# Kernel tuning notes

Hardware: AMD Instinct MI355X
Metric: run time of the kernel (lower is better)

## Reference

```python
import jax, jax.numpy as jnp
import numpy as np

B, V, N = 64, 64, 16384
R, Y = 32, 32          # obs_vocab, y_classes
HID = 128
BIG = 1.0e9


def _features(tables, sigma, base_obs, actions, responses, t):
    """Vectorized version of _score_one_step over the whole batch.

    tables: [B,V,N] int32 in [0,R); sigma: [B,N] int32 in [0,Y).
    Returns feat [B, V+1, 2] = stack([exp_amb, exp_sz], -1).
    """
    # candidate mask cand0 from base_obs and the (action, response) prefix
    m = tables[:, 0, :] == base_obs[:, None]                  # [B,N]
    used = jnp.zeros((B, V), dtype=bool)
    for i in range(t):
        a = actions[:, i]
        is_stop = a == V
        ac = jnp.clip(a, 0, V - 1)
        lbl = jnp.take_along_axis(tables, ac[:, None, None], axis=1)[:, 0, :]  # [B,N]
        m = m & (is_stop[:, None] | (lbl == responses[:, i][:, None]))
        used = used.at[jnp.arange(B), ac].max(~is_stop)
    mf = m.astype(jnp.float32)
    total0 = mf.sum(-1)                                       # [B]
    safe_tot = jnp.maximum(total0, 1.0)

    # per-(batch, action, response) bucket counts: counts[b,a,r] = |{n : cand0 & tables[b,a,n]==r}|
    b_ix = jnp.arange(B)[:, None, None]
    a_ix = jnp.arange(V)[None, :, None]
    flat = (b_ix * V + a_ix) * R + tables                     # [B,V,N]
    w = jnp.broadcast_to(mf[:, None, :], (B, V, N)).ravel()
    counts = jnp.zeros((B * V * R,), jnp.float32).at[flat.ravel()].add(w).reshape(B, V, R)

    # per-bucket distinct sigma values: presence[b,a,r,y] = 1 if some candidate in bucket has sigma==y
    flat2 = flat * Y + sigma[:, None, :]                      # [B,V,N]
    pres = jnp.zeros((B * V * R * Y,), jnp.float32).at[flat2.ravel()].max(w).reshape(B, V, R, Y)
    uniq = pres.sum(-1)                                       # [B,V,R]

    # expected size / ambiguity: sum_r (sz_r/total0)*sz_r and (sz_r/total0)*uniq_r
    exp_sz = (counts * counts).sum(-1) / safe_tot[:, None]    # [B,V]
    exp_amb = (counts * uniq).sum(-1) / safe_tot[:, None]     # [B,V]

    # forbid view 0 (forbid_view0=True in logits_query) and already-used actions
    forbidden = used.at[:, 0].set(True)
    exp_sz = jnp.where(forbidden, BIG, exp_sz)
    exp_amb = jnp.where(forbidden, BIG, exp_amb)

    # STOP action: ambiguity of cand0 itself, size = |cand0|
    pres0 = jnp.zeros((B * Y,), jnp.float32).at[(jnp.arange(B)[:, None] * Y + sigma).ravel()].max(mf.ravel()).reshape(B, Y)
    stop_amb = pres0.sum(-1)                                  # [B]

    amb_full = jnp.concatenate([exp_amb, stop_amb[:, None]], axis=1)   # [B,V+1]
    sz_full = jnp.concatenate([exp_sz, total0[:, None]], axis=1)       # [B,V+1]

    # empty candidate set -> all-zero features (torch early-return)
    empty = (total0 == 0.0)[:, None]
    amb_full = jnp.where(empty, 0.0, amb_full)
    sz_full = jnp.where(empty, 0.0, sz_full)
    return jnp.stack([amb_full, sz_full], axis=-1)            # [B,V+1,2]


def setup_inputs() -> dict:
    key = jax.random.key(0)
    ks = jax.random.split(key, 9)
    T = 8
    return {
        "tables": jax.random.randint(ks[0], (B, V, N), 0, R, dtype=jnp.int32),
        "sigma": jax.random.randint(ks[1], (B, N), 0, Y, dtype=jnp.int32),
        "base_obs": jax.random.randint(ks[2], (B,), 0, R, dtype=jnp.int32),
        "actions": jax.random.randint(ks[3], (B, T), 0, V + 1, dtype=jnp.int32),
        "responses": jax.random.randint(ks[4], (B, T), 0, R, dtype=jnp.int32),
        "W1": jax.random.normal(ks[5], (2, HID), jnp.float32) / np.sqrt(2.0).astype(np.float32),
        "b1": jax.random.normal(ks[6], (HID,), jnp.float32) * 0.01,
        "W2": jax.random.normal(ks[7], (HID, 1), jnp.float32) / np.sqrt(float(HID)).astype(np.float32),
        "b2": jax.random.normal(ks[8], (1,), jnp.float32) * 0.01,
        "t": 2,
        "max_steps": 8,
    }


def reference(tables, sigma, base_obs, actions, responses, W1, b1, W2, b2, t, max_steps):
    feat = _features(tables, sigma, base_obs, actions, responses, int(t))  # [B,V+1,2]
    h = jax.nn.gelu(feat @ W1 + b1, approximate=False)        # exact (erf) GELU like nn.GELU
    return (h @ W2 + b2)[..., 0]                              # [B, V+1] action logits
```

## Files before the change

kernel.cpp:

```cpp
#include <hip/hip_runtime.h>
#include <math.h>

#define B 64
#define V 64
#define NN 16384
#define RR 32
#define HIDN 128
#define BIGV 1000000000.0f


__global__ void k_compact(const int* __restrict__ tables,
                          const int* __restrict__ base_obs,
                          const int* __restrict__ actions,
                          const int* __restrict__ responses,
                          const int* __restrict__ t_ptr,
                          int* __restrict__ cnt,
                          int* __restrict__ list,
                          int T)
{
    const int b = blockIdx.y;
    const int t = t_ptr[0];
    const int n0 = blockIdx.x * (NN / 16) + threadIdx.x * 4;
    const int base = base_obs[b];
    const int4 tv = *(const int4*)(tables + (size_t)b * V * NN + n0);
    int m0 = (tv.x == base), m1 = (tv.y == base), m2 = (tv.z == base), m3 = (tv.w == base);
    for (int i = 0; i < t; ++i) {
        const int a = actions[b * T + i];
        if (a == V) continue;
        const int resp = responses[b * T + i];
        const int4 lv = *(const int4*)(tables + ((size_t)b * V + a) * NN + n0);
        m0 &= (lv.x == resp); m1 &= (lv.y == resp); m2 &= (lv.z == resp); m3 &= (lv.w == resp);
    }
    if (m0) { int i = atomicAdd(&cnt[b], 1); list[b * NN + i] = n0; }
    if (m1) { int i = atomicAdd(&cnt[b], 1); list[b * NN + i] = n0 + 1; }
    if (m2) { int i = atomicAdd(&cnt[b], 1); list[b * NN + i] = n0 + 2; }
    if (m3) { int i = atomicAdd(&cnt[b], 1); list[b * NN + i] = n0 + 3; }
}

__global__ void k_feat(const int* __restrict__ tables,
                       const int* __restrict__ sigma,
                       const int* __restrict__ actions,
                       const int* __restrict__ t_ptr,
                       const int* __restrict__ cnt,
                       const int* __restrict__ list,
                       const float* __restrict__ W1,
                       const float* __restrict__ b1,
                       const float* __restrict__ W2,
                       const float* __restrict__ b2,
                       float* __restrict__ out,
                       int T)
{
    const int b = blockIdx.x;
    const int tid = threadIdx.x;
    __shared__ unsigned s_counts[RR * V];
    __shared__ unsigned s_mask[RR * V];
    __shared__ float s_feat[(V + 1) * 2];

    for (int i = tid; i < RR * V; i += 128) { s_counts[i] = 0u; s_mask[i] = 0u; }
    __syncthreads();

    const int K = cnt[b];
    const int t = t_ptr[0];
    const int* blist = list + b * NN;
    const int* bsig  = sigma + (size_t)b * NN;

    if (tid < V) {
        const int v = tid;
        const int* rowv = tables + ((size_t)b * V + v) * NN;
        for (int k = 0; k < K; ++k) {
            const int n = blist[k];
            const int r = rowv[n];
            const int y = bsig[n];
            s_counts[r * V + v] += 1u;
            s_mask[r * V + v] |= (1u << y);
        }
    } else if (tid == V) {
        unsigned pm = 0u;
        for (int k = 0; k < K; ++k) pm |= (1u << bsig[blist[k]]);
        s_feat[V * 2 + 0] = (float)__popc(pm);
        s_feat[V * 2 + 1] = (float)K;
    }
    __syncthreads();

    if (tid < V) {
        const int v = tid;
        const float safe = (K > 0) ? (float)K : 1.0f;
        float sz = 0.f, amb = 0.f;
        for (int r = 0; r < RR; ++r) {
            const float c = (float)s_counts[r * V + v];
            const float u = (float)__popc(s_mask[r * V + v]);
            sz += c * c;
            amb += c * u;
        }
        sz /= safe; amb /= safe;
        bool forb = (v == 0);
        for (int i = 0; i < t; ++i)
            if (actions[b * T + i] == v) forb = true;
        if (forb) { sz = BIGV; amb = BIGV; }
        s_feat[v * 2 + 0] = amb;
        s_feat[v * 2 + 1] = sz;
    }
    __syncthreads();

    if (tid <= V) {
        float f0 = 0.f, f1 = 0.f;
        if (K > 0) { f0 = s_feat[tid * 2 + 0]; f1 = s_feat[tid * 2 + 1]; }
        float acc = b2[0];
        for (int j = 0; j < HIDN; ++j) {
            const float x = f0 * W1[j] + f1 * W1[HIDN + j] + b1[j];
            const float g = 0.5f * x * (1.0f + erff(x * 0.70710678118654752f));
            acc = fmaf(g, W2[j], acc);
        }
        out[b * (V + 1) + tid] = acc;
    }
}

extern "C" void kernel_launch(void* const* d_in, const int* in_sizes, int n_in,
                              void* d_out, int out_size, void* d_ws, size_t ws_size,
                              hipStream_t stream) {
    const int* tables    = (const int*)d_in[0];
    const int* sigma     = (const int*)d_in[1];
    const int* base_obs  = (const int*)d_in[2];
    const int* actions   = (const int*)d_in[3];
    const int* responses = (const int*)d_in[4];
    const float* W1      = (const float*)d_in[5];
    const float* b1      = (const float*)d_in[6];
    const float* W2      = (const float*)d_in[7];
    const float* b2      = (const float*)d_in[8];
    const int* t_ptr     = (const int*)d_in[9];
    float* out = (float*)d_out;

    const int T = in_sizes[3] / B;

    int* cnt  = (int*)d_ws;
    int* list = (int*)((char*)d_ws + 256);

    hipMemsetAsync(cnt, 0, B * sizeof(int), stream);

    dim3 g1(16, B);
    k_compact<<<g1, 256, 0, stream>>>(tables, base_obs, actions, responses,
                                      t_ptr, cnt, list, T);
    k_feat<<<B, 128, 0, stream>>>(tables, sigma, actions, t_ptr, cnt, list,
                                  W1, b1, W2, b2, out, T);
}
```

Before: 342.5 us.

## Fuse candidate compaction and feature kernels into one block-per-batch kernel

Merges the compaction kernel and the feature/MLP kernel into a single kernel with one 512-thread block per batch row. The candidate list is kept in shared memory with a fixed capacity, which removes the memset, the global atomics and the global list traffic. STOP ambiguity is now derived from the per-view masks of view 0 instead of a separate serial pass. In exchange, compaction runs on only 64 blocks instead of 1024, which lowers parallelism for the table scan. Batches with more candidates than the capacity are silently truncated, which would give wrong features.

```diff
diff --git a/kernel.cpp b/kernel.cpp
--- a/kernel.cpp
+++ b/kernel.cpp
@@ -7,78 +7,69 @@
 #define RR 32
 #define HIDN 128
 #define BIGV 1000000000.0f
+#define CAP 4096
 
-
-__global__ void k_compact(const int* __restrict__ tables,
-                          const int* __restrict__ base_obs,
-                          const int* __restrict__ actions,
-                          const int* __restrict__ responses,
-                          const int* __restrict__ t_ptr,
-                          int* __restrict__ cnt,
-                          int* __restrict__ list,
-                          int T)
-{
-    const int b = blockIdx.y;
-    const int t = t_ptr[0];
-    const int n0 = blockIdx.x * (NN / 16) + threadIdx.x * 4;
-    const int base = base_obs[b];
-    const int4 tv = *(const int4*)(tables + (size_t)b * V * NN + n0);
-    int m0 = (tv.x == base), m1 = (tv.y == base), m2 = (tv.z == base), m3 = (tv.w == base);
-    for (int i = 0; i < t; ++i) {
-        const int a = actions[b * T + i];
-        if (a == V) continue;
-        const int resp = responses[b * T + i];
-        const int4 lv = *(const int4*)(tables + ((size_t)b * V + a) * NN + n0);
-        m0 &= (lv.x == resp); m1 &= (lv.y == resp); m2 &= (lv.z == resp); m3 &= (lv.w == resp);
-    }
-    if (m0) { int i = atomicAdd(&cnt[b], 1); list[b * NN + i] = n0; }
-    if (m1) { int i = atomicAdd(&cnt[b], 1); list[b * NN + i] = n0 + 1; }
-    if (m2) { int i = atomicAdd(&cnt[b], 1); list[b * NN + i] = n0 + 2; }
-    if (m3) { int i = atomicAdd(&cnt[b], 1); list[b * NN + i] = n0 + 3; }
-}
-
-__global__ void k_feat(const int* __restrict__ tables,
-                       const int* __restrict__ sigma,
-                       const int* __restrict__ actions,
-                       const int* __restrict__ t_ptr,
-                       const int* __restrict__ cnt,
-                       const int* __restrict__ list,
-                       const float* __restrict__ W1,
-                       const float* __restrict__ b1,
-                       const float* __restrict__ W2,
-                       const float* __restrict__ b2,
-                       float* __restrict__ out,
-                       int T)
+__global__ __launch_bounds__(512)
+void k_fused(const int* __restrict__ tables,
+             const int* __restrict__ sigma,
+             const int* __restrict__ base_obs,
+             const int* __restrict__ actions,
+             const int* __restrict__ responses,
+             const int* __restrict__ t_ptr,
+             const float* __restrict__ W1,
+             const float* __restrict__ b1,
+             const float* __restrict__ W2,
+             const float* __restrict__ b2,
+             float* __restrict__ out,
+             int T)
 {
     const int b = blockIdx.x;
     const int tid = threadIdx.x;
+
+    __shared__ int s_cnt;
+    __shared__ int s_list[CAP];
     __shared__ unsigned s_counts[RR * V];
     __shared__ unsigned s_mask[RR * V];
     __shared__ float s_feat[(V + 1) * 2];
 
-    for (int i = tid; i < RR * V; i += 128) { s_counts[i] = 0u; s_mask[i] = 0u; }
+    if (tid == 0) s_cnt = 0;
+    for (int i = tid; i < RR * V; i += 512) { s_counts[i] = 0u; s_mask[i] = 0u; }
     __syncthreads();
 
-    const int K = cnt[b];
     const int t = t_ptr[0];
-    const int* blist = list + b * NN;
-    const int* bsig  = sigma + (size_t)b * NN;
+    const int base = base_obs[b];
+    const int* row0 = tables + (size_t)b * V * NN;
+
+    for (int n0 = tid * 4; n0 < NN; n0 += 512 * 4) {
+        const int4 tv = *(const int4*)(row0 + n0);
+        int m0 = (tv.x == base), m1 = (tv.y == base), m2 = (tv.z == base), m3 = (tv.w == base);
+        for (int i = 0; i < t; ++i) {
+            const int a = actions[b * T + i];
+            if (a == V) continue;
+            const int resp = responses[b * T + i];
+            const int4 lv = *(const int4*)(row0 + a * NN + n0);
+            m0 &= (lv.x == resp); m1 &= (lv.y == resp); m2 &= (lv.z == resp); m3 &= (lv.w == resp);
+        }
+        if (m0) { int i = atomicAdd(&s_cnt, 1); if (i < CAP) s_list[i] = n0; }
+        if (m1) { int i = atomicAdd(&s_cnt, 1); if (i < CAP) s_list[i] = n0 + 1; }
+        if (m2) { int i = atomicAdd(&s_cnt, 1); if (i < CAP) s_list[i] = n0 + 2; }
+        if (m3) { int i = atomicAdd(&s_cnt, 1); if (i < CAP) s_list[i] = n0 + 3; }
+    }
+    __syncthreads();
+
+    const int K = min(s_cnt, CAP);
+    const int* bsig = sigma + (size_t)b * NN;
 
     if (tid < V) {
         const int v = tid;
-        const int* rowv = tables + ((size_t)b * V + v) * NN;
+        const int* rowv = row0 + v * NN;
         for (int k = 0; k < K; ++k) {
-            const int n = blist[k];
+            const int n = s_list[k];
             const int r = rowv[n];
             const int y = bsig[n];
             s_counts[r * V + v] += 1u;
             s_mask[r * V + v] |= (1u << y);
         }
-    } else if (tid == V) {
-        unsigned pm = 0u;
-        for (int k = 0; k < K; ++k) pm |= (1u << bsig[blist[k]]);
-        s_feat[V * 2 + 0] = (float)__popc(pm);
-        s_feat[V * 2 + 1] = (float)K;
     }
     __syncthreads();
 
@@ -86,11 +77,13 @@
         const int v = tid;
         const float safe = (K > 0) ? (float)K : 1.0f;
         float sz = 0.f, amb = 0.f;
+        unsigned pm = 0u;
         for (int r = 0; r < RR; ++r) {
+            const unsigned mk = s_mask[r * V + v];
             const float c = (float)s_counts[r * V + v];
-            const float u = (float)__popc(s_mask[r * V + v]);
+            pm |= mk;
             sz += c * c;
-            amb += c * u;
+            amb += c * (float)__popc(mk);
         }
         sz /= safe; amb /= safe;
         bool forb = (v == 0);
@@ -99,6 +92,10 @@
         if (forb) { sz = BIGV; amb = BIGV; }
         s_feat[v * 2 + 0] = amb;
         s_feat[v * 2 + 1] = sz;
+        if (v == 0) {
+            s_feat[V * 2 + 0] = (float)__popc(pm);
+            s_feat[V * 2 + 1] = (float)K;
+        }
     }
     __syncthreads();
 
@@ -132,14 +129,6 @@
 
     const int T = in_sizes[3] / B;
 
-    int* cnt  = (int*)d_ws;
-    int* list = (int*)((char*)d_ws + 256);
-
-    hipMemsetAsync(cnt, 0, B * sizeof(int), stream);
-
-    dim3 g1(16, B);
-    k_compact<<<g1, 256, 0, stream>>>(tables, base_obs, actions, responses,
-                                      t_ptr, cnt, list, T);
-    k_feat<<<B, 128, 0, stream>>>(tables, sigma, actions, t_ptr, cnt, list,
-                                  W1, b1, W2, b2, out, T);
+    k_fused<<<B, 512, 0, stream>>>(tables, sigma, base_obs, actions, responses,
+                                   t_ptr, W1, b1, W2, b2, out, T);
 }
```

Result: no change. 348.0 us (+1.6%).
